# Kernel optimization log

Hardware: AMD Instinct MI355X
Metric: run time of the kernel (lower is better)

The kernel has to match this reference:

```python
import jax, jax.numpy as jnp
import numpy as np

NUM_HEADS = 4
NUM_POINTS = 8


def deform_attn_3d(q, value, ref, Hf, Wf, Wv, bv, Wo, bo, Wa, ba):
    # q: (BS,N,C)  value: (BS,Hf*Wf,C)  ref: (BS,N,D,2) normalized (x,y) in [0,1]
    BS, N, C = q.shape
    H, P = NUM_HEADS, NUM_POINTS
    D = ref.shape[2]
    c = C // H
    # value projection, split heads: (BS,H,M,c)
    v = (value @ Wv + bv).reshape(BS, Hf * Wf, H, c).transpose(0, 2, 1, 3)
    # sampling offsets and attention weights from the query
    off = (q @ Wo + bo).reshape(BS, N, H, P, 2)
    attn = jax.nn.softmax((q @ Wa + ba).reshape(BS, N, H, P), axis=-1)
    # normalize offsets by (W,H); distribute P points over D z-anchors (P//D per anchor)
    norm = jnp.array([Wf, Hf], dtype=q.dtype)
    off = off.reshape(BS, N, H, P // D, D, 2) / norm
    loc = (ref[:, :, None, None, :, :] + off).reshape(BS, N, H, P, 2)
    # grid_sample(align_corners=False, padding=zeros): pixel = loc*size - 0.5
    x = loc[..., 0] * Wf - 0.5
    y = loc[..., 1] * Hf - 0.5
    x0f = jnp.floor(x)
    y0f = jnp.floor(y)
    lx = x - x0f
    ly = y - y0f
    x0 = x0f.astype(jnp.int32)
    y0 = y0f.astype(jnp.int32)

    def tohead(a):  # (BS,N,H,P) -> (BS,H,N*P)
        return a.transpose(0, 2, 1, 3).reshape(BS, H, N * P)

    def gather(yy, xx):
        valid = ((xx >= 0) & (xx < Wf) & (yy >= 0) & (yy < Hf)).astype(q.dtype)
        idx = jnp.clip(yy, 0, Hf - 1) * Wf + jnp.clip(xx, 0, Wf - 1)
        g = jnp.take_along_axis(v, tohead(idx)[..., None], axis=2)  # (BS,H,N*P,c)
        return g * tohead(valid)[..., None]

    out = (gather(y0, x0) * tohead((1 - lx) * (1 - ly))[..., None]
           + gather(y0, x0 + 1) * tohead(lx * (1 - ly))[..., None]
           + gather(y0 + 1, x0) * tohead((1 - lx) * ly)[..., None]
           + gather(y0 + 1, x0 + 1) * tohead(lx * ly)[..., None])
    out = (out * tohead(attn)[..., None]).reshape(BS, H, N, P, c).sum(3)  # (BS,H,N,c)
    return out.transpose(0, 2, 1, 3).reshape(BS, N, C)


def spatial_cross_attention(query, query_pos, value, reference_points_cam, bev_mask,
                            Hf, Wf, Wv, bv, Wo, bo, Wa, ba, Wout, bout):
    # query/query_pos: (B,N,C); value: (S,M,B,C); ref: (S,B,N,D,2); bev_mask: (S,B,N,D)
    B, N, C = query.shape
    S, M = value.shape[0], value.shape[1]
    D = reference_points_cam.shape[3]
    q = query + query_pos
    # broadcast queries over cameras (mask-equivalent of the torch rebatch/compaction):
    # deformable attention is per-query independent, so computing all queries per cam
    # and masking invalid ones is the same math as rebatch+scatter.
    q_all = jnp.broadcast_to(q[:, None], (B, S, N, C)).reshape(B * S, N, C)
    v_all = value.transpose(2, 0, 1, 3).reshape(B * S, M, C)
    ref = reference_points_cam.transpose(1, 0, 2, 3, 4).reshape(B * S, N, D, 2)
    out = deform_attn_3d(q_all, v_all, ref, Hf, Wf, Wv, bv, Wo, bo, Wa, ba)
    out = out.reshape(B, S, N, C)
    mask_q = (bev_mask.sum(-1) > 0).astype(query.dtype)  # (S,B,N): query hits this cam
    slots = (out * mask_q.transpose(1, 0, 2)[..., None]).sum(1)  # (B,N,C)
    count = jnp.maximum(mask_q.sum(0), 1.0)  # (B,N) clamp(min=1)
    slots = slots / count[..., None]
    # output_proj, dropout (eval -> identity), residual with original query
    return slots @ Wout + bout + query


def setup_inputs() -> dict:
    B, S, N, Z, C = 1, 6, 16384, 8, 128
    Hf, Wf = 28, 50
    H, P = NUM_HEADS, NUM_POINTS
    rng = jax.random.key(0)
    ks = jax.random.split(rng, 12)
    return {
        "query": jax.random.normal(ks[0], (B, N, C), jnp.float32),
        "query_pos": 0.1 * jax.random.normal(ks[1], (B, N, C), jnp.float32),
        "value": jax.random.normal(ks[2], (S, Hf * Wf, B, C), jnp.float32),
        "reference_points_cam": jax.random.uniform(ks[3], (S, B, N, Z, 2), jnp.float32),
        "bev_mask": jax.random.randint(ks[4], (S, B, N, Z), 0, 2).astype(bool),
        "Wv": 0.02 * jax.random.normal(ks[5], (C, C), jnp.float32),
        "bv": jnp.zeros((C,), jnp.float32),
        "Wo": 0.02 * jax.random.normal(ks[6], (C, H * P * 2), jnp.float32),
        "bo": 0.5 * jax.random.normal(ks[7], (H * P * 2,), jnp.float32),
        "Wa": 0.02 * jax.random.normal(ks[8], (C, H * P), jnp.float32),
        "ba": jnp.zeros((H * P,), jnp.float32),
        "Wout": 0.02 * jax.random.normal(ks[9], (C, C), jnp.float32),
        "bout": jnp.zeros((C,), jnp.float32),
        "Hf": Hf,
        "Wf": Wf,
    }


def reference(query, query_pos, value, reference_points_cam, bev_mask,
              Wv, bv, Wo, bo, Wa, ba, Wout, bout, Hf, Wf):
    return spatial_cross_attention(query, query_pos, value, reference_points_cam, bev_mask,
                                   Hf, Wf, Wv, bv, Wo, bo, Wa, ba, Wout, bout)
```

## Files before the change

kernel.cpp:

```cpp
#include <hip/hip_runtime.h>

#define N_Q   16384
#define C_DIM 128
#define S_CAM 6
#define M_VAL 1400
#define D_Z   8
#define HF    28
#define WF    50
#define QPB   8

typedef float f32x2 __attribute__((ext_vector_type(2)));

__device__ __forceinline__ bool mask_any(const unsigned char* __restrict__ mask,
                                         int mflag, size_t mbase){
  if(mflag==0){
    int any=0;
    #pragma unroll
    for(int d=0;d<D_Z;d++) any |= mask[mbase+d];
    return any!=0;
  } else if(mflag==1){
    const int* mp = (const int*)mask;  int any=0;
    #pragma unroll
    for(int d=0;d<D_Z;d++) any |= mp[mbase+d];
    return any!=0;
  } else {
    const long long* mp = (const long long*)mask;  long long any=0;
    #pragma unroll
    for(int d=0;d<D_Z;d++) any |= mp[mbase+d];
    return any!=0;
  }
}

__device__ __forceinline__ void corner_acc(const uint4 cv, const float wgt,
                                           f32x2* __restrict__ acc2){
  const f32x2 w2 = {wgt, wgt};
  const unsigned dw[4] = {cv.x, cv.y, cv.z, cv.w};
  #pragma unroll
  for(int j=0;j<4;j++){
    acc2[j*2+0] += w2 * __builtin_amdgcn_cvt_pk_f32_fp8(dw[j], false);
    acc2[j*2+1] += w2 * __builtin_amdgcn_cvt_pk_f32_fp8(dw[j], true);
  }
}

__global__ __launch_bounds__(256)
void value_proj_kernel(const float* __restrict__ value,
                       const float* __restrict__ Wv,
                       const float* __restrict__ bv,
                       unsigned char* __restrict__ v8,
                       const unsigned char* __restrict__ mask,
                       int* __restrict__ flag){
  __shared__ float tile[8][C_DIM];
  __shared__ int s_cntA, s_cntB;
  const int tid = threadIdx.x;
  const int col = tid & 127;
  const int rh  = tid >> 7;
  const int r0  = blockIdx.x * 8;
  if(blockIdx.x==0 && tid==0){ s_cntA=0; s_cntB=0; }
  {
    const float4* src = (const float4*)(value + (size_t)r0*C_DIM);
    ((float4*)&tile[0][0])[tid] = src[tid];
  }
  __syncthreads();
  float acc[4];
  const float bias = bv[col];
  #pragma unroll
  for(int r=0;r<4;r++) acc[r]=bias;
  for(int k=0;k<C_DIM;k+=4){
    const float w0 = Wv[(k+0)*C_DIM + col];
    const float w1 = Wv[(k+1)*C_DIM + col];
    const float w2 = Wv[(k+2)*C_DIM + col];
    const float w3 = Wv[(k+3)*C_DIM + col];
    #pragma unroll
    for(int r=0;r<4;r++){
      const float4 t = *(const float4*)&tile[rh*4+r][k];
      acc[r] += t.x*w0 + t.y*w1 + t.z*w2 + t.w*w3;
    }
  }
  #pragma unroll
  for(int r=0;r<4;r++){
    const int pk = __builtin_amdgcn_cvt_pk_fp8_f32(acc[r], acc[r], 0, false);
    v8[(size_t)(r0+rh*4+r)*C_DIM + col] = (unsigned char)(pk & 0xff);
  }
  if(blockIdx.x==0){
    int a=0, b=0;
    for(int i=tid;i<1024;i+=256){
      const unsigned char v = mask[i];
      if(((i&3)!=0) && v) a=1;
      if(((i&7)==4) && v) b=1;
    }
    if(a) atomicOr(&s_cntA,1);
    if(b) atomicOr(&s_cntB,1);
    __syncthreads();
    if(tid==0) flag[0] = s_cntA ? 0 : (s_cntB ? 1 : 2);
  }
}

__global__ __launch_bounds__(256)
void fused_deform_kernel(const unsigned char* __restrict__ v8,
                         const float* __restrict__ query,
                         const float* __restrict__ query_pos,
                         const float* __restrict__ Wo, const float* __restrict__ bo,
                         const float* __restrict__ Wa, const float* __restrict__ ba,
                         const float* __restrict__ ref,
                         const unsigned char* __restrict__ mask,
                         const int* __restrict__ flag,
                         const float* __restrict__ Wout,
                         const float* __restrict__ bout,
                         float* __restrict__ out){
  __shared__ float  qs[QPB][C_DIM+4];
  __shared__ float  offs[QPB][68];
  __shared__ float  attns[QPB][36];
  __shared__ float  logits[QPB][36];
  __shared__ float2 refs[QPB][S_CAM*D_Z+1];
  __shared__ int    activ[QPB][S_CAM];
  __shared__ float  cinv[QPB];

  const int tid = threadIdx.x;
  const int n0  = blockIdx.x * QPB;
  const int mflag = flag[0];
  const int qi = tid >> 5;
  const int l  = tid & 31;

  float2 rpre0, rpre1;
  {
    const int q0 = tid/48, r0 = tid%48;
    rpre0 = ((const float2*)ref)[((size_t)(r0>>3)*N_Q + (n0+q0))*D_Z + (r0&7)];
    if(tid < 128){
      const int e1 = tid + 256;
      const int q1 = e1/48, r1 = e1%48;
      rpre1 = ((const float2*)ref)[((size_t)(r1>>3)*N_Q + (n0+q1))*D_Z + (r1&7)];
    }
  }

  {
    const float4* qa = (const float4*)(query     + (size_t)n0*C_DIM);
    const float4* qb = (const float4*)(query_pos + (size_t)n0*C_DIM);
    const int r = tid >> 5, c4 = tid & 31;
    const float4 A = qa[tid], B = qb[tid];
    *(float4*)&qs[r][c4*4] = make_float4(A.x+B.x, A.y+B.y, A.z+B.z, A.w+B.w);
  }
  __syncthreads();

  {
    float ao0 = bo[l*2+0], ao1 = bo[l*2+1];
    float aa  = ba[l];
    for(int k=0;k<C_DIM;k++){
      const float qv = qs[qi][k];
      const float2 wo = *(const float2*)&Wo[k*64 + l*2];
      const float  wa = Wa[k*32 + l];
      ao0 += qv*wo.x; ao1 += qv*wo.y; aa += qv*wa;
    }
    offs[qi][l*2+0] = ao0;  offs[qi][l*2+1] = ao1;
    logits[qi][l] = aa;
  }
  {
    refs[tid/48][tid%48] = rpre0;
    if(tid < 128){
      const int e1 = tid + 256;
      refs[e1/48][e1%48] = rpre1;
    }
  }
  if(tid < QPB*S_CAM){
    const int q2 = tid / S_CAM, s = tid % S_CAM;
    activ[q2][s] = mask_any(mask, mflag, ((size_t)s*N_Q + (n0+q2))*D_Z) ? 1 : 0;
  }
  __syncthreads();
  if(tid < QPB*4){
    const int q2 = tid >> 2, h = tid & 3;
    const float* L = &logits[q2][h*8];
    float mx = L[0];
    #pragma unroll
    for(int p=1;p<8;p++) mx = fmaxf(mx, L[p]);
    float e[8], ssum = 0.f;
    #pragma unroll
    for(int p=0;p<8;p++){ e[p] = __expf(L[p]-mx); ssum += e[p]; }
    const float inv = 1.f/ssum;
    #pragma unroll
    for(int p=0;p<8;p++) attns[q2][h*8+p] = e[p]*inv;
  } else if(tid >= 256-QPB){
    const int q2 = tid - (256-QPB);
    int c = 0;
    #pragma unroll
    for(int s=0;s<S_CAM;s++) c += activ[q2][s];
    cinv[q2] = 1.f / fmaxf((float)c, 1.f);
  }
  __syncthreads();

  const int pg  = l >> 4;
  const int sg  = (l >> 3) & 1;
  const int ll  = l & 7;
  const int gch = ll*16;
  const int gh  = ll >> 1;
  f32x2 acc2[8];
  #pragma unroll
  for(int i=0;i<8;i++) acc2[i] = (f32x2){0.f, 0.f};

  for(int s=sg*3; s<sg*3+3; s++){
    if(!activ[qi][s]) continue;
    const unsigned char* vb = v8 + (size_t)s*M_VAL*C_DIM + gch;
    #pragma unroll 2
    for(int pp=0;pp<4;pp++){
      const int p = pg*4 + pp;
      const float2 r2 = refs[qi][s*8+p];
      const float ox = offs[qi][gh*16+p*2+0];
      const float oy = offs[qi][gh*16+p*2+1];
      const float x = fmaf(r2.x, (float)WF, ox - 0.5f);
      const float y = fmaf(r2.y, (float)HF, oy - 0.5f);
      const float x0f = floorf(x), y0f = floorf(y);
      const float fx = x - x0f,    fy = y - y0f;
      const int x0 = (int)x0f, y0 = (int)y0f;
      const int x1 = x0+1,     y1 = y0+1;
      const float at = attns[qi][gh*8+p];
      const float wx0 = (x0>=0 && x0<WF) ? (1.f-fx) : 0.f;
      const float wx1 = (x1>=0 && x1<WF) ? fx       : 0.f;
      const float wy0 = ((y0>=0 && y0<HF) ? (1.f-fy) : 0.f) * at;
      const float wy1 = ((y1>=0 && y1<HF) ? fy       : 0.f) * at;
      const int x0c = min(max(x0,0), WF-1), x1c = min(max(x1,0), WF-1);
      const int y0c = min(max(y0,0), HF-1), y1c = min(max(y1,0), HF-1);
      const float w00 = wx0*wy0, w01 = wx1*wy0, w10 = wx0*wy1, w11 = wx1*wy1;
      const uint4 c00 = *(const uint4*)(vb + (size_t)(y0c*WF+x0c)*C_DIM);
      const uint4 c01 = *(const uint4*)(vb + (size_t)(y0c*WF+x1c)*C_DIM);
      const uint4 c10 = *(const uint4*)(vb + (size_t)(y1c*WF+x0c)*C_DIM);
      const uint4 c11 = *(const uint4*)(vb + (size_t)(y1c*WF+x1c)*C_DIM);
      corner_acc(c00, w00, acc2);
      corner_acc(c01, w01, acc2);
      corner_acc(c10, w10, acc2);
      corner_acc(c11, w11, acc2);
    }
  }

  float* accf = (float*)acc2;
  #pragma unroll
  for(int i=0;i<16;i++) accf[i] += __shfl_xor(accf[i], 16);
  #pragma unroll
  for(int i=0;i<16;i++) accf[i] += __shfl_xor(accf[i], 8);
  if(l < 8){
    const float inv = cinv[qi];
    #pragma unroll
    for(int i=0;i<4;i++)
      *(float4*)&qs[qi][gch+i*4] = make_float4(accf[i*4+0]*inv, accf[i*4+1]*inv,
                                               accf[i*4+2]*inv, accf[i*4+3]*inv);
  }

  {
    const int c0 = l*4;
    const int n  = n0 + qi;
    const float4 bA = *(const float4*)&bout[c0];
    const float4 rA = *(const float4*)&query[(size_t)n*C_DIM + c0];
    float o0=bA.x+rA.x, o1=bA.y+rA.y, o2=bA.z+rA.z, o3=bA.w+rA.w;
    for(int k=0;k<C_DIM;k++){
      const float sv = qs[qi][k];
      const float4 wA = *(const float4*)&Wout[(size_t)k*C_DIM + c0];
      o0 += sv*wA.x; o1 += sv*wA.y; o2 += sv*wA.z; o3 += sv*wA.w;
    }
    *(float4*)&out[(size_t)n*C_DIM + c0] = make_float4(o0,o1,o2,o3);
  }
}

extern "C" void kernel_launch(void* const* d_in, const int* in_sizes, int n_in,
                              void* d_out, int out_size, void* d_ws, size_t ws_size,
                              hipStream_t stream){
  const float* query     = (const float*)d_in[0];
  const float* query_pos = (const float*)d_in[1];
  const float* value     = (const float*)d_in[2];
  const float* ref       = (const float*)d_in[3];
  const unsigned char* mask = (const unsigned char*)d_in[4];
  const float* Wv   = (const float*)d_in[5];
  const float* bv   = (const float*)d_in[6];
  const float* Wo   = (const float*)d_in[7];
  const float* bo   = (const float*)d_in[8];
  const float* Wa   = (const float*)d_in[9];
  const float* ba   = (const float*)d_in[10];
  const float* Wout = (const float*)d_in[11];
  const float* bout = (const float*)d_in[12];
  float* out = (float*)d_out;

  int* flag = (int*)d_ws;
  unsigned char* v8 = (unsigned char*)((char*)d_ws + 64);

  value_proj_kernel<<<(S_CAM*M_VAL)/8, 256, 0, stream>>>(value, Wv, bv, v8, mask, flag);
  fused_deform_kernel<<<N_Q/QPB, 256, 0, stream>>>(v8, query, query_pos,
                                                   Wo, bo, Wa, ba, ref, mask, flag,
                                                   Wout, bout, out);
}
```

Baseline: 189.8 us.

## Split K across half-waves and register-block two queries in projection GEMVs

Rewrites the three small matmuls (value projection, offset/attention-logit projection, output projection) so that each thread covers half of the K dimension and computes several rows or queries at once. Partial sums are combined through LDS in the value projection and through cross-half-wave shuffles in the fused kernel. Each weight element loaded from global memory is now reused across two queries or eight rows, and the loads are vectorized as float4. The cost is more registers per thread, extra shuffle or LDS reduction steps, and some idle lanes (cg >= 24) in the offset projection.

```diff
diff --git a/kernel.cpp b/kernel.cpp
--- a/kernel.cpp
+++ b/kernel.cpp
@@ -50,10 +50,11 @@
                        const unsigned char* __restrict__ mask,
                        int* __restrict__ flag){
   __shared__ float tile[8][C_DIM];
+  __shared__ float part[8][C_DIM];
   __shared__ int s_cntA, s_cntB;
   const int tid = threadIdx.x;
-  const int col = tid & 127;
-  const int rh  = tid >> 7;
+  const int c   = tid & 127;
+  const int kh  = tid >> 7;
   const int r0  = blockIdx.x * 8;
   if(blockIdx.x==0 && tid==0){ s_cntA=0; s_cntB=0; }
   {
@@ -61,25 +62,40 @@
     ((float4*)&tile[0][0])[tid] = src[tid];
   }
   __syncthreads();
-  float acc[4];
-  const float bias = bv[col];
-  #pragma unroll
-  for(int r=0;r<4;r++) acc[r]=bias;
-  for(int k=0;k<C_DIM;k+=4){
-    const float w0 = Wv[(k+0)*C_DIM + col];
-    const float w1 = Wv[(k+1)*C_DIM + col];
-    const float w2 = Wv[(k+2)*C_DIM + col];
-    const float w3 = Wv[(k+3)*C_DIM + col];
-    #pragma unroll
-    for(int r=0;r<4;r++){
-      const float4 t = *(const float4*)&tile[rh*4+r][k];
-      acc[r] += t.x*w0 + t.y*w1 + t.z*w2 + t.w*w3;
-    }
-  }
-  #pragma unroll
-  for(int r=0;r<4;r++){
-    const int pk = __builtin_amdgcn_cvt_pk_fp8_f32(acc[r], acc[r], 0, false);
-    v8[(size_t)(r0+rh*4+r)*C_DIM + col] = (unsigned char)(pk & 0xff);
+  float acc[8];
+  {
+    const float bias = kh ? 0.f : bv[c];
+    #pragma unroll
+    for(int r=0;r<8;r++) acc[r]=bias;
+  }
+  {
+    const float* Wp = Wv + (size_t)kh*64*C_DIM + c;
+    const int k00 = kh*64;
+    for(int k0=0;k0<64;k0+=4){
+      const float w0 = Wp[0];
+      const float w1 = Wp[C_DIM];
+      const float w2 = Wp[2*C_DIM];
+      const float w3 = Wp[3*C_DIM];
+      #pragma unroll
+      for(int r=0;r<8;r++){
+        const float4 t = *(const float4*)&tile[r][k00+k0];
+        acc[r] += t.x*w0 + t.y*w1 + t.z*w2 + t.w*w3;
+      }
+      Wp += 4*C_DIM;
+    }
+  }
+  if(kh){
+    #pragma unroll
+    for(int r=0;r<8;r++) part[r][c] = acc[r];
+  }
+  __syncthreads();
+  if(!kh){
+    #pragma unroll
+    for(int r=0;r<8;r++){
+      const float v = acc[r] + part[r][c];
+      const int pk = __builtin_amdgcn_cvt_pk_fp8_f32(v, v, 0, false);
+      v8[(size_t)(r0+r)*C_DIM + c] = (unsigned char)(pk & 0xff);
+    }
   }
   if(blockIdx.x==0){
     int a=0, b=0;
@@ -120,6 +136,10 @@
   const int mflag = flag[0];
   const int qi = tid >> 5;
   const int l  = tid & 31;
+  const int wi = tid >> 6;
+  const int ln = tid & 63;
+  const int kh = ln >> 5;
+  const int cg = ln & 31;
 
   float2 rpre0, rpre1;
   {
@@ -142,16 +162,48 @@
   __syncthreads();
 
   {
-    float ao0 = bo[l*2+0], ao1 = bo[l*2+1];
-    float aa  = ba[l];
-    for(int k=0;k<C_DIM;k++){
-      const float qv = qs[qi][k];
-      const float2 wo = *(const float2*)&Wo[k*64 + l*2];
-      const float  wa = Wa[k*32 + l];
-      ao0 += qv*wo.x; ao1 += qv*wo.y; aa += qv*wa;
-    }
-    offs[qi][l*2+0] = ao0;  offs[qi][l*2+1] = ao1;
-    logits[qi][l] = aa;
+    const int qA = 2*wi, qB = qA+1;
+    float a0=0.f,a1=0.f,a2=0.f,a3=0.f, b0=0.f,b1=0.f,b2=0.f,b3=0.f;
+    if(cg < 24){
+      const float* Wp; int stride;
+      if(cg < 16){ Wp = Wo + cg*4;      stride = 64; }
+      else       { Wp = Wa + (cg-16)*4; stride = 32; }
+      if(kh==0){
+        const float4 bia = (cg<16) ? *(const float4*)&bo[cg*4]
+                                   : *(const float4*)&ba[(cg-16)*4];
+        a0=bia.x; a1=bia.y; a2=bia.z; a3=bia.w;
+        b0=bia.x; b1=bia.y; b2=bia.z; b3=bia.w;
+      }
+      Wp += (size_t)kh*64*stride;
+      const int k00 = kh*64;
+      for(int k0=0;k0<64;k0+=4){
+        const float4 qa = *(const float4*)&qs[qA][k00+k0];
+        const float4 qb = *(const float4*)&qs[qB][k00+k0];
+        const float4 w0 = *(const float4*)&Wp[0];
+        const float4 w1 = *(const float4*)&Wp[stride];
+        const float4 w2 = *(const float4*)&Wp[2*stride];
+        const float4 w3 = *(const float4*)&Wp[3*stride];
+        a0 += qa.x*w0.x + qa.y*w1.x + qa.z*w2.x + qa.w*w3.x;
+        a1 += qa.x*w0.y + qa.y*w1.y + qa.z*w2.y + qa.w*w3.y;
+        a2 += qa.x*w0.z + qa.y*w1.z + qa.z*w2.z + qa.w*w3.z;
+        a3 += qa.x*w0.w + qa.y*w1.w + qa.z*w2.w + qa.w*w3.w;
+        b0 += qb.x*w0.x + qb.y*w1.x + qb.z*w2.x + qb.w*w3.x;
+        b1 += qb.x*w0.y + qb.y*w1.y + qb.z*w2.y + qb.w*w3.y;
+        b2 += qb.x*w0.z + qb.y*w1.z + qb.z*w2.z + qb.w*w3.z;
+        b3 += qb.x*w0.w + qb.y*w1.w + qb.z*w2.w + qb.w*w3.w;
+        Wp += 4*stride;
+      }
+    }
+    a0 += __shfl_xor(a0,32); a1 += __shfl_xor(a1,32);
+    a2 += __shfl_xor(a2,32); a3 += __shfl_xor(a3,32);
+    b0 += __shfl_xor(b0,32); b1 += __shfl_xor(b1,32);
+    b2 += __shfl_xor(b2,32); b3 += __shfl_xor(b3,32);
+    if(cg < 24){
+      const float4 r = kh ? make_float4(b0,b1,b2,b3) : make_float4(a0,a1,a2,a3);
+      const int q = qA + kh;
+      if(cg < 16) *(float4*)&offs[q][cg*4] = r;
+      else        *(float4*)&logits[q][(cg-16)*4] = r;
+    }
   }
   {
     refs[tid/48][tid%48] = rpre0;
@@ -243,17 +295,42 @@
   }
 
   {
-    const int c0 = l*4;
-    const int n  = n0 + qi;
-    const float4 bA = *(const float4*)&bout[c0];
-    const float4 rA = *(const float4*)&query[(size_t)n*C_DIM + c0];
-    float o0=bA.x+rA.x, o1=bA.y+rA.y, o2=bA.z+rA.z, o3=bA.w+rA.w;
-    for(int k=0;k<C_DIM;k++){
-      const float sv = qs[qi][k];
-      const float4 wA = *(const float4*)&Wout[(size_t)k*C_DIM + c0];
-      o0 += sv*wA.x; o1 += sv*wA.y; o2 += sv*wA.z; o3 += sv*wA.w;
-    }
-    *(float4*)&out[(size_t)n*C_DIM + c0] = make_float4(o0,o1,o2,o3);
+    const int qA = 2*wi, qB = qA+1;
+    const int c0 = cg*4;
+    float o0=0.f,o1=0.f,o2=0.f,o3=0.f, p0=0.f,p1=0.f,p2=0.f,p3=0.f;
+    if(kh==0){
+      const float4 bb = *(const float4*)&bout[c0];
+      const float4 rA = *(const float4*)&query[(size_t)(n0+qA)*C_DIM + c0];
+      const float4 rB = *(const float4*)&query[(size_t)(n0+qB)*C_DIM + c0];
+      o0=bb.x+rA.x; o1=bb.y+rA.y; o2=bb.z+rA.z; o3=bb.w+rA.w;
+      p0=bb.x+rB.x; p1=bb.y+rB.y; p2=bb.z+rB.z; p3=bb.w+rB.w;
+    }
+    const float* Wp = Wout + (size_t)kh*64*C_DIM + c0;
+    const int k00 = kh*64;
+    for(int k0=0;k0<64;k0+=4){
+      const float4 sa = *(const float4*)&qs[qA][k00+k0];
+      const float4 sb = *(const float4*)&qs[qB][k00+k0];
+      const float4 w0 = *(const float4*)&Wp[0];
+      const float4 w1 = *(const float4*)&Wp[C_DIM];
+      const float4 w2 = *(const float4*)&Wp[2*C_DIM];
+      const float4 w3 = *(const float4*)&Wp[3*C_DIM];
+      o0 += sa.x*w0.x + sa.y*w1.x + sa.z*w2.x + sa.w*w3.x;
+      o1 += sa.x*w0.y + sa.y*w1.y + sa.z*w2.y + sa.w*w3.y;
+      o2 += sa.x*w0.z + sa.y*w1.z + sa.z*w2.z + sa.w*w3.z;
+      o3 += sa.x*w0.w + sa.y*w1.w + sa.z*w2.w + sa.w*w3.w;
+      p0 += sb.x*w0.x + sb.y*w1.x + sb.z*w2.x + sb.w*w3.x;
+      p1 += sb.x*w0.y + sb.y*w1.y + sb.z*w2.y + sb.w*w3.y;
+      p2 += sb.x*w0.z + sb.y*w1.z + sb.z*w2.z + sb.w*w3.z;
+      p3 += sb.x*w0.w + sb.y*w1.w + sb.z*w2.w + sb.w*w3.w;
+      Wp += 4*C_DIM;
+    }
+    o0 += __shfl_xor(o0,32); o1 += __shfl_xor(o1,32);
+    o2 += __shfl_xor(o2,32); o3 += __shfl_xor(o3,32);
+    p0 += __shfl_xor(p0,32); p1 += __shfl_xor(p1,32);
+    p2 += __shfl_xor(p2,32); p3 += __shfl_xor(p3,32);
+    const int n = n0 + qA + kh;
+    const float4 r = kh ? make_float4(p0,p1,p2,p3) : make_float4(o0,o1,o2,o3);
+    *(float4*)&out[(size_t)n*C_DIM + c0] = r;
   }
 }
 
```

Result: faster. 166.0 us (-12.5%).
